# Performance work log

Hardware: AMD Instinct MI355X
Metric: run time of the kernel (lower is better)

## Reference

```python
import jax, jax.numpy as jnp
import numpy as np

N, F, HOPS, HID, NCLS = 100000, 128, 8, 256, 64

def prelu(x, a):
    return jnp.where(x >= 0, x, a * x)

def setup_inputs() -> dict:
    key = jax.random.key(0)
    ks = jax.random.split(key, 8)
    w = lambda i, shape: (jax.random.normal(ks[i], shape, dtype=jnp.float32) * 0.02)
    return {
        "feats": jax.random.normal(ks[0], (HOPS, N, F), dtype=jnp.float32),
        # lr_jk_ref: Dense(HOPS*F, HID) -> PReLU(a_jk) -> Dense(HID, HID)
        "W_jk1": w(1, (HOPS * F, HID)), "b_jk1": jnp.zeros((HID,), jnp.float32),
        "W_jk2": w(2, (HID, HID)),      "b_jk2": jnp.zeros((HID,), jnp.float32),
        # PReLU params (nn.PReLU default init 0.25): FFN-internal, module-level, output-FFN
        "a_jk": jnp.float32(0.25), "a_main": jnp.float32(0.25), "a_out": jnp.float32(0.25),
        # lr_att: Linear(HID + F, 1), split into the jk_ref part and the per-hop x part
        "w_att_ref": w(3, (HID,)), "w_att_x": w(4, (F,)), "b_att": jnp.zeros((), jnp.float32),
        # lr_output: Dense(F, HID) -> PReLU(a_out) -> Dense(HID, NCLS)
        "W_o1": w(5, (F, HID)),  "b_o1": jnp.zeros((HID,), jnp.float32),
        "W_o2": w(6, (HID, NCLS)), "b_o2": jnp.zeros((NCLS,), jnp.float32),
    }

def reference(feats, W_jk1, b_jk1, W_jk2, b_jk2, a_jk, a_main, a_out,
              w_att_ref, w_att_x, b_att, W_o1, b_o1, W_o2, b_o2):
    # feats: [HOPS, N, F]; dropouts are identity (rates = 0 / eval mode)
    n = feats.shape[1]
    # torch.cat(input_list, dim=1) -> [N, HOPS*F]
    concat = jnp.transpose(feats, (1, 0, 2)).reshape(n, -1)
    # lr_jk_ref (FeedForwardNetII, n_layers=2): Dense -> PReLU -> Dense, then module PReLU
    h = prelu(concat @ W_jk1 + b_jk1, a_jk)
    jk_ref = prelu(h @ W_jk2 + b_jk2, a_main)              # [N, HID]
    # attention scores: sigmoid(Linear(cat(jk_ref, x_i))) for each hop i, vectorized
    s_ref = jk_ref @ w_att_ref                              # [N]
    s_x = jnp.einsum('hnf,f->nh', feats, w_att_x)           # [N, HOPS]
    scores = jax.nn.sigmoid(s_x + s_ref[:, None] + b_att)   # [N, HOPS]
    Wsm = jax.nn.softmax(scores, axis=1)                    # softmax over hops
    # weighted multi-hop aggregation: sum_i W[:,i] * x_i
    agg = jnp.einsum('nh,hnf->nf', Wsm, feats)              # [N, F]
    # lr_output (FeedForwardNetII, n_layers=2): Dense -> PReLU -> Dense
    out = prelu(agg @ W_o1 + b_o1, a_out) @ W_o2 + b_o2     # [N, NCLS]
    return out
```

## Files before the change

### kernel.cpp

```cpp
#include <hip/hip_runtime.h>
#include <hip/hip_bf16.h>
#include <cstdint>
#include <cstddef>

#define N_F 128
#define N_HOPS 8
#define N_HID 256
#define N_CLS 64

typedef __bf16 bf16;
typedef __attribute__((ext_vector_type(8))) __bf16 bf16x8;
typedef __attribute__((ext_vector_type(4))) float f32x4;

__device__ inline f32x4 mfma16(bf16x8 a, bf16x8 b, f32x4 c) {
    return __builtin_amdgcn_mfma_f32_16x16x32_bf16(a, b, c, 0, 0, 0);
}

typedef const __attribute__((address_space(1))) unsigned int guint;
typedef __attribute__((address_space(3))) unsigned int luint;
__device__ __forceinline__ void gl_lds16(const void* g, void* l) {
    __builtin_amdgcn_global_load_lds((guint*)g, (luint*)l, 16, 0, 0);
}

__device__ inline void pack_one(const float* __restrict__ s, bf16* __restrict__ d,
                                int NC, int ntn, int idx) {
    const int lane = idx & 63;
    const int f = idx >> 6;
    const int kt = f / ntn, nt = f - kt * ntn;
    const int krow = kt * 32 + ((lane >> 4) << 3);
    const int col = nt * 16 + (lane & 15);
    const float* ss = s + (size_t)krow * NC + col;
    bf16* dd = d + ((size_t)f * 64 + lane) * 8;
#pragma unroll
    for (int j = 0; j < 8; ++j) dd[j] = (bf16)ss[(size_t)j * NC];
}

__global__ void pack_weights(const float* __restrict__ W1, const float* __restrict__ W2,
                             const float* __restrict__ O1, const float* __restrict__ O2,
                             bf16* p1, bf16* p2, bf16* p3, bf16* p4) {
    int i = blockIdx.x * 256 + threadIdx.x;
    if (i < 32768) { pack_one(W1, p1, 256, 16, i); return; }
    i -= 32768;
    if (i < 8192)  { pack_one(W2, p2, 256, 16, i); return; }
    i -= 8192;
    if (i < 4096)  { pack_one(O1, p3, 256, 16, i); return; }
    i -= 4096;
    if (i < 2048)  { pack_one(O2, p4, 64, 4, i); return; }
}

__global__ __launch_bounds__(256) void k1_kernel(
    const float* __restrict__ feats, const bf16* __restrict__ w1p, const bf16* __restrict__ w2p,
    const float* __restrict__ b1, const float* __restrict__ b2,
    const float* __restrict__ a_jk_p, const float* __restrict__ a_main_p,
    const float* __restrict__ wref, const float* __restrict__ wax,
    const float* __restrict__ batt_p,
    float* __restrict__ wsm, int N)
{
    union __align__(16) U1 {
        struct { bf16 A[2048]; bf16 B[8192]; } s;
        bf16 H[64 * 264];
    };
    __shared__ U1 u;
    __shared__ float sx[64 * 8];
    __shared__ float sref[64];

    const int t = threadIdx.x;
    const int lane = t & 63;
    const int wc = t >> 6;
    const int row0 = blockIdx.x * 64;

    for (int i = t; i < 64 * 8; i += 256) sx[i] = 0.f;
    if (t < 64) sref[t] = 0.f;
    __syncthreads();

    const int srow = t & 63;
    const int sc = t >> 6;
    const int grow = min(row0 + srow, N - 1);

    f32x4 acc[4][4] = {};
    float pacc = 0.f;

    for (int kt = 0; kt < 32; ++kt) {
        const int h = kt >> 2;
        const int f0 = ((kt & 3) << 5) + (sc << 3);
        const float* srcp = feats + ((size_t)h * N + grow) * N_F + f0;
        const float4 v0 = *(const float4*)srcp;
        const float4 v1 = *(const float4*)(srcp + 4);
        pacc += v0.x * wax[f0]     + v0.y * wax[f0 + 1] + v0.z * wax[f0 + 2] + v0.w * wax[f0 + 3]
              + v1.x * wax[f0 + 4] + v1.y * wax[f0 + 5] + v1.z * wax[f0 + 6] + v1.w * wax[f0 + 7];
        if ((kt & 3) == 3) { atomicAdd(&sx[srow * 8 + h], pacc); pacc = 0.f; }
        bf16x8 av;
        av[0] = (bf16)v0.x; av[1] = (bf16)v0.y; av[2] = (bf16)v0.z; av[3] = (bf16)v0.w;
        av[4] = (bf16)v1.x; av[5] = (bf16)v1.y; av[6] = (bf16)v1.z; av[7] = (bf16)v1.w;
        *(bf16x8*)&u.s.A[((((srow >> 4) << 6) + (sc << 4) + (srow & 15))) << 3] = av;
        const bf16* bsrc = w1p + (size_t)kt * 8192;
#pragma unroll
        for (int r = 0; r < 4; ++r)
            gl_lds16(bsrc + r * 2048 + t * 8, &u.s.B[r * 2048 + t * 8]);
        __syncthreads();
        bf16x8 af[4], bfr[4];
#pragma unroll
        for (int i = 0; i < 4; ++i) af[i] = *(bf16x8*)&u.s.A[((i << 6) + lane) << 3];
#pragma unroll
        for (int j = 0; j < 4; ++j) bfr[j] = *(bf16x8*)&u.s.B[(((wc << 2) + j) * 64 + lane) << 3];
#pragma unroll
        for (int i = 0; i < 4; ++i)
#pragma unroll
            for (int j = 0; j < 4; ++j)
                acc[i][j] = mfma16(af[i], bfr[j], acc[i][j]);
        __syncthreads();
    }

    const float ajk = *a_jk_p;
#pragma unroll
    for (int j = 0; j < 4; ++j) {
        const int colg = (wc << 6) + (j << 4) + (lane & 15);
        const float bias = b1[colg];
#pragma unroll
        for (int i = 0; i < 4; ++i)
#pragma unroll
            for (int r = 0; r < 4; ++r) {
                const int row = (i << 4) + ((lane >> 4) << 2) + r;
                float v = acc[i][j][r] + bias;
                v = v >= 0.f ? v : ajk * v;
                u.H[row * 264 + colg] = (bf16)v;
            }
    }
    __syncthreads();

    f32x4 acc2[4][4] = {};
    for (int kt = 0; kt < 8; ++kt) {
        bf16x8 af[4], bfr[4];
#pragma unroll
        for (int i = 0; i < 4; ++i)
            af[i] = *(bf16x8*)&u.H[((i << 4) + (lane & 15)) * 264 + (kt << 5) + ((lane >> 4) << 3)];
#pragma unroll
        for (int j = 0; j < 4; ++j)
            bfr[j] = *(const bf16x8*)&w2p[((size_t)((kt << 4) + (wc << 2) + j) * 64 + lane) * 8];
#pragma unroll
        for (int i = 0; i < 4; ++i)
#pragma unroll
            for (int j = 0; j < 4; ++j)
                acc2[i][j] = mfma16(af[i], bfr[j], acc2[i][j]);
    }

    const float amain = *a_main_p;
    float pr[4][4] = {};
#pragma unroll
    for (int j = 0; j < 4; ++j) {
        const int colg = (wc << 6) + (j << 4) + (lane & 15);
        const float bias = b2[colg];
        const float wr_ = wref[colg];
#pragma unroll
        for (int i = 0; i < 4; ++i)
#pragma unroll
            for (int r = 0; r < 4; ++r) {
                float v = acc2[i][j][r] + bias;
                v = v >= 0.f ? v : amain * v;
                pr[i][r] += v * wr_;
            }
    }
#pragma unroll
    for (int m = 1; m < 16; m <<= 1)
#pragma unroll
        for (int i = 0; i < 4; ++i)
#pragma unroll
            for (int r = 0; r < 4; ++r)
                pr[i][r] += __shfl_xor(pr[i][r], m, 64);
    if ((lane & 15) == 0) {
#pragma unroll
        for (int i = 0; i < 4; ++i)
#pragma unroll
            for (int r = 0; r < 4; ++r)
                atomicAdd(&sref[(i << 4) + ((lane >> 4) << 2) + r], pr[i][r]);
    }
    __syncthreads();

    if (t < 64) {
        const int rg = row0 + t;
        if (rg < N) {
            const float sr = sref[t] + *batt_p;
            float e[8], mx = -1e30f;
#pragma unroll
            for (int h = 0; h < 8; ++h) {
                const float s = 1.f / (1.f + expf(-(sx[t * 8 + h] + sr)));
                e[h] = s; mx = fmaxf(mx, s);
            }
            float sum = 0.f;
#pragma unroll
            for (int h = 0; h < 8; ++h) { e[h] = expf(e[h] - mx); sum += e[h]; }
            const float inv = 1.f / sum;
#pragma unroll
            for (int h = 0; h < 8; ++h) wsm[(size_t)rg * 8 + h] = e[h] * inv;
        }
    }
}

__global__ __launch_bounds__(256) void k2_kernel(
    const float* __restrict__ feats, const float* __restrict__ wsm,
    const bf16* __restrict__ o1p, const bf16* __restrict__ o2p,
    const float* __restrict__ bo1, const float* __restrict__ a_out_p,
    const float* __restrict__ bo2, float* __restrict__ out, int N)
{
    union __align__(16) U2 {
        bf16 AG[64 * 136];
        bf16 HO[64 * 264];
    };
    __shared__ U2 u;
    __shared__ float wsl[512];

    const int t = threadIdx.x;
    const int lane = t & 63;
    const int cg = t >> 6;
    const int row0 = blockIdx.x * 64;

    for (int i = t; i < 512; i += 256) {
        const int rg = min(row0 + (i >> 3), N - 1);
        wsl[i] = wsm[(size_t)rg * 8 + (i & 7)];
    }
    __syncthreads();

    {
        const int r = t >> 2;
        const int c = t & 3;
        const int rg = min(row0 + r, N - 1);
        f32x4 a4[8] = {};
#pragma unroll
        for (int h = 0; h < 8; ++h) {
            const float wgt = wsl[r * 8 + h];
            const f32x4* p4 = (const f32x4*)(feats + ((size_t)h * N + rg) * N_F + c * 32);
#pragma unroll
            for (int q = 0; q < 8; ++q) a4[q] += wgt * p4[q];
        }
#pragma unroll
        for (int q2 = 0; q2 < 4; ++q2) {
            bf16x8 av;
#pragma unroll
            for (int e = 0; e < 4; ++e) {
                av[e] = (bf16)a4[q2 * 2][e];
                av[4 + e] = (bf16)a4[q2 * 2 + 1][e];
            }
            *(bf16x8*)&u.AG[r * 136 + c * 32 + q2 * 8] = av;
        }
    }
    __syncthreads();

    f32x4 acc3[4][4] = {};
    for (int kt = 0; kt < 4; ++kt) {
        bf16x8 af[4], bfr[4];
#pragma unroll
        for (int i = 0; i < 4; ++i)
            af[i] = *(bf16x8*)&u.AG[((i << 4) + (lane & 15)) * 136 + (kt << 5) + ((lane >> 4) << 3)];
#pragma unroll
        for (int j = 0; j < 4; ++j)
            bfr[j] = *(const bf16x8*)&o1p[((size_t)((kt << 4) + (cg << 2) + j) * 64 + lane) * 8];
#pragma unroll
        for (int i = 0; i < 4; ++i)
#pragma unroll
            for (int j = 0; j < 4; ++j)
                acc3[i][j] = mfma16(af[i], bfr[j], acc3[i][j]);
    }
    __syncthreads();

    const float aout = *a_out_p;
#pragma unroll
    for (int j = 0; j < 4; ++j) {
        const int colg = (cg << 6) + (j << 4) + (lane & 15);
        const float bias = bo1[colg];
#pragma unroll
        for (int i = 0; i < 4; ++i)
#pragma unroll
            for (int r = 0; r < 4; ++r) {
                const int row = (i << 4) + ((lane >> 4) << 2) + r;
                float v = acc3[i][j][r] + bias;
                v = v >= 0.f ? v : aout * v;
                u.HO[row * 264 + colg] = (bf16)v;
            }
    }
    __syncthreads();

    f32x4 acc4[4] = {};
    for (int kt = 0; kt < 8; ++kt) {
        const bf16x8 b = *(const bf16x8*)&o2p[((size_t)((kt << 2) + cg) * 64 + lane) * 8];
#pragma unroll
        for (int i = 0; i < 4; ++i) {
            const bf16x8 a = *(bf16x8*)&u.HO[((i << 4) + (lane & 15)) * 264 + (kt << 5) + ((lane >> 4) << 3)];
            acc4[i] = mfma16(a, b, acc4[i]);
        }
    }
    {
        const int colg = (cg << 4) + (lane & 15);
        const float bv = bo2[colg];
#pragma unroll
        for (int i = 0; i < 4; ++i)
#pragma unroll
            for (int r = 0; r < 4; ++r) {
                const int rg = row0 + (i << 4) + ((lane >> 4) << 2) + r;
                if (rg < N) out[(size_t)rg * 64 + colg] = acc4[i][r] + bv;
            }
    }
}

extern "C" void kernel_launch(void* const* d_in, const int* in_sizes, int n_in,
                              void* d_out, int out_size, void* d_ws, size_t ws_size,
                              hipStream_t stream) {
    const float* feats  = (const float*)d_in[0];
    const float* W1     = (const float*)d_in[1];
    const float* b1     = (const float*)d_in[2];
    const float* W2     = (const float*)d_in[3];
    const float* b2     = (const float*)d_in[4];
    const float* a_jk   = (const float*)d_in[5];
    const float* a_main = (const float*)d_in[6];
    const float* a_out  = (const float*)d_in[7];
    const float* wref   = (const float*)d_in[8];
    const float* wax    = (const float*)d_in[9];
    const float* batt   = (const float*)d_in[10];
    const float* O1     = (const float*)d_in[11];
    const float* bo1    = (const float*)d_in[12];
    const float* O2     = (const float*)d_in[13];
    const float* bo2    = (const float*)d_in[14];

    const int N = in_sizes[0] / (N_HOPS * N_F);

    char* ws = (char*)d_ws;
    bf16* p1 = (bf16*)ws;
    bf16* p2 = (bf16*)(ws + 524288);
    bf16* p3 = (bf16*)(ws + 655360);
    bf16* p4 = (bf16*)(ws + 720896);
    float* wsm = (float*)(ws + 753664);

    pack_weights<<<184, 256, 0, stream>>>(W1, W2, O1, O2, p1, p2, p3, p4);
    const int nb = (N + 63) / 64;
    k1_kernel<<<nb, 256, 0, stream>>>(feats, p1, p2, b1, b2, a_jk, a_main,
                                      wref, wax, batt, wsm, N);
    k2_kernel<<<nb, 256, 0, stream>>>(feats, wsm, p3, p4, bo1, a_out, bo2,
                                      (float*)d_out, N);
}
```

Before: 771.9 us.

## Fuse attention and output kernels, double-buffer W1 tiles, repartition first GEMM by row

Merges the two per-row kernels into one, so the softmax hop weights stay in shared memory and the second pass over feats can hit cache soon after the first. The first GEMM now gives each wave 16 rows across all 256 columns, with A fragments loaded straight into registers. W1 tiles are double-buffered in LDS with the next tile prefetched, which drops one barrier per iteration. Hop scores are reduced with shuffles instead of shared atomics, and the aggregation loop prefetches the next hop. In exchange, each wave now reads all 16 B fragments per step, and register pressure and LDS footprint grow, which may lower occupancy.

```diff
diff --git a/kernel.cpp b/kernel.cpp
--- a/kernel.cpp
+++ b/kernel.cpp
@@ -48,107 +48,122 @@
     if (i < 2048)  { pack_one(O2, p4, 64, 4, i); return; }
 }
 
-__global__ __launch_bounds__(256) void k1_kernel(
+__global__ __launch_bounds__(256) void fused_kernel(
     const float* __restrict__ feats, const bf16* __restrict__ w1p, const bf16* __restrict__ w2p,
+    const bf16* __restrict__ o1p, const bf16* __restrict__ o2p,
     const float* __restrict__ b1, const float* __restrict__ b2,
     const float* __restrict__ a_jk_p, const float* __restrict__ a_main_p,
     const float* __restrict__ wref, const float* __restrict__ wax,
     const float* __restrict__ batt_p,
-    float* __restrict__ wsm, int N)
+    const float* __restrict__ bo1, const float* __restrict__ a_out_p,
+    const float* __restrict__ bo2, float* __restrict__ out, int N)
 {
-    union __align__(16) U1 {
-        struct { bf16 A[2048]; bf16 B[8192]; } s;
+    union __align__(16) U {
+        bf16 B[2][8192];
         bf16 H[64 * 264];
+        bf16 AG[64 * 136];
+        bf16 HO[64 * 264];
     };
-    __shared__ U1 u;
+    __shared__ U u;
     __shared__ float sx[64 * 8];
     __shared__ float sref[64];
 
     const int t = threadIdx.x;
     const int lane = t & 63;
-    const int wc = t >> 6;
+    const int wv = t >> 6;
     const int row0 = blockIdx.x * 64;
-
-    for (int i = t; i < 64 * 8; i += 256) sx[i] = 0.f;
+    const int rA = lane & 15;
+    const int cA = lane >> 4;
+
     if (t < 64) sref[t] = 0.f;
-    __syncthreads();
-
-    const int srow = t & 63;
-    const int sc = t >> 6;
-    const int grow = min(row0 + srow, N - 1);
-
-    f32x4 acc[4][4] = {};
+
+    const int growA = min(row0 + (wv << 4) + rA, N - 1);
+    const float* arow = feats + (size_t)growA * N_F + (cA << 3);
+    const size_t hopstride = (size_t)N * N_F;
+
+    f32x4 acc[16] = {};
     float pacc = 0.f;
 
+    float4 v0 = *(const float4*)(arow);
+    float4 v1 = *(const float4*)(arow + 4);
+#pragma unroll
+    for (int q = 0; q < 4; ++q)
+        gl_lds16(w1p + q * 2048 + t * 8, &u.B[0][q * 2048 + t * 8]);
+    __syncthreads();
+
+#pragma unroll 2
     for (int kt = 0; kt < 32; ++kt) {
-        const int h = kt >> 2;
-        const int f0 = ((kt & 3) << 5) + (sc << 3);
-        const float* srcp = feats + ((size_t)h * N + grow) * N_F + f0;
-        const float4 v0 = *(const float4*)srcp;
-        const float4 v1 = *(const float4*)(srcp + 4);
-        pacc += v0.x * wax[f0]     + v0.y * wax[f0 + 1] + v0.z * wax[f0 + 2] + v0.w * wax[f0 + 3]
-              + v1.x * wax[f0 + 4] + v1.y * wax[f0 + 5] + v1.z * wax[f0 + 6] + v1.w * wax[f0 + 7];
-        if ((kt & 3) == 3) { atomicAdd(&sx[srow * 8 + h], pacc); pacc = 0.f; }
-        bf16x8 av;
-        av[0] = (bf16)v0.x; av[1] = (bf16)v0.y; av[2] = (bf16)v0.z; av[3] = (bf16)v0.w;
-        av[4] = (bf16)v1.x; av[5] = (bf16)v1.y; av[6] = (bf16)v1.z; av[7] = (bf16)v1.w;
-        *(bf16x8*)&u.s.A[((((srow >> 4) << 6) + (sc << 4) + (srow & 15))) << 3] = av;
-        const bf16* bsrc = w1p + (size_t)kt * 8192;
-#pragma unroll
-        for (int r = 0; r < 4; ++r)
-            gl_lds16(bsrc + r * 2048 + t * 8, &u.s.B[r * 2048 + t * 8]);
+        const int cur = kt & 1;
+        float4 v0n, v1n;
+        if (kt < 31) {
+            const int kn = kt + 1;
+            const float* np = arow + (size_t)(kn >> 2) * hopstride + ((kn & 3) << 5);
+            v0n = *(const float4*)np;
+            v1n = *(const float4*)(np + 4);
+            const bf16* bsrc = w1p + (size_t)kn * 8192;
+#pragma unroll
+            for (int q = 0; q < 4; ++q)
+                gl_lds16(bsrc + q * 2048 + t * 8, &u.B[cur ^ 1][q * 2048 + t * 8]);
+        }
+        const int f0 = ((kt & 3) << 5) + (cA << 3);
+        const float4 wx0 = *(const float4*)&wax[f0];
+        const float4 wx1 = *(const float4*)&wax[f0 + 4];
+        pacc += v0.x * wx0.x + v0.y * wx0.y + v0.z * wx0.z + v0.w * wx0.w
+              + v1.x * wx1.x + v1.y * wx1.y + v1.z * wx1.z + v1.w * wx1.w;
+        if ((kt & 3) == 3) {
+            pacc += __shfl_xor(pacc, 16, 64);
+            pacc += __shfl_xor(pacc, 32, 64);
+            if (lane < 16) sx[(((wv << 4) + lane) << 3) + (kt >> 2)] = pacc;
+            pacc = 0.f;
+        }
+        bf16x8 af;
+        af[0] = (bf16)v0.x; af[1] = (bf16)v0.y; af[2] = (bf16)v0.z; af[3] = (bf16)v0.w;
+        af[4] = (bf16)v1.x; af[5] = (bf16)v1.y; af[6] = (bf16)v1.z; af[7] = (bf16)v1.w;
+#pragma unroll
+        for (int j = 0; j < 16; ++j) {
+            const bf16x8 bfr = *(const bf16x8*)&u.B[cur][((j << 6) + lane) << 3];
+            acc[j] = mfma16(af, bfr, acc[j]);
+        }
+        if (kt < 31) { v0 = v0n; v1 = v1n; }
         __syncthreads();
-        bf16x8 af[4], bfr[4];
-#pragma unroll
-        for (int i = 0; i < 4; ++i) af[i] = *(bf16x8*)&u.s.A[((i << 6) + lane) << 3];
-#pragma unroll
-        for (int j = 0; j < 4; ++j) bfr[j] = *(bf16x8*)&u.s.B[(((wc << 2) + j) * 64 + lane) << 3];
-#pragma unroll
-        for (int i = 0; i < 4; ++i)
-#pragma unroll
-            for (int j = 0; j < 4; ++j)
-                acc[i][j] = mfma16(af[i], bfr[j], acc[i][j]);
-        __syncthreads();
     }
 
     const float ajk = *a_jk_p;
 #pragma unroll
-    for (int j = 0; j < 4; ++j) {
-        const int colg = (wc << 6) + (j << 4) + (lane & 15);
+    for (int j = 0; j < 16; ++j) {
+        const int colg = (j << 4) + rA;
         const float bias = b1[colg];
 #pragma unroll
-        for (int i = 0; i < 4; ++i)
-#pragma unroll
-            for (int r = 0; r < 4; ++r) {
-                const int row = (i << 4) + ((lane >> 4) << 2) + r;
-                float v = acc[i][j][r] + bias;
-                v = v >= 0.f ? v : ajk * v;
-                u.H[row * 264 + colg] = (bf16)v;
-            }
+        for (int r = 0; r < 4; ++r) {
+            const int row = (wv << 4) + (cA << 2) + r;
+            float v = acc[j][r] + bias;
+            v = v >= 0.f ? v : ajk * v;
+            u.H[row * 264 + colg] = (bf16)v;
+        }
     }
     __syncthreads();
 
     f32x4 acc2[4][4] = {};
     for (int kt = 0; kt < 8; ++kt) {
-        bf16x8 af[4], bfr[4];
-#pragma unroll
-        for (int i = 0; i < 4; ++i)
-            af[i] = *(bf16x8*)&u.H[((i << 4) + (lane & 15)) * 264 + (kt << 5) + ((lane >> 4) << 3)];
+        bf16x8 af2[4], bfr[4];
+#pragma unroll
+        for (int i = 0; i < 4; ++i)
+            af2[i] = *(bf16x8*)&u.H[((i << 4) + rA) * 264 + (kt << 5) + (cA << 3)];
 #pragma unroll
         for (int j = 0; j < 4; ++j)
-            bfr[j] = *(const bf16x8*)&w2p[((size_t)((kt << 4) + (wc << 2) + j) * 64 + lane) * 8];
+            bfr[j] = *(const bf16x8*)&w2p[((size_t)((kt << 4) + (wv << 2) + j) * 64 + lane) * 8];
 #pragma unroll
         for (int i = 0; i < 4; ++i)
 #pragma unroll
             for (int j = 0; j < 4; ++j)
-                acc2[i][j] = mfma16(af[i], bfr[j], acc2[i][j]);
+                acc2[i][j] = mfma16(af2[i], bfr[j], acc2[i][j]);
     }
 
     const float amain = *a_main_p;
     float pr[4][4] = {};
 #pragma unroll
     for (int j = 0; j < 4; ++j) {
-        const int colg = (wc << 6) + (j << 4) + (lane & 15);
+        const int colg = (wv << 6) + (j << 4) + rA;
         const float bias = b2[colg];
         const float wr_ = wref[colg];
 #pragma unroll
@@ -167,56 +182,29 @@
 #pragma unroll
             for (int r = 0; r < 4; ++r)
                 pr[i][r] += __shfl_xor(pr[i][r], m, 64);
-    if ((lane & 15) == 0) {
+    if (rA == 0) {
 #pragma unroll
         for (int i = 0; i < 4; ++i)
 #pragma unroll
             for (int r = 0; r < 4; ++r)
-                atomicAdd(&sref[(i << 4) + ((lane >> 4) << 2) + r], pr[i][r]);
+                atomicAdd(&sref[(i << 4) + (cA << 2) + r], pr[i][r]);
     }
     __syncthreads();
 
     if (t < 64) {
-        const int rg = row0 + t;
-        if (rg < N) {
-            const float sr = sref[t] + *batt_p;
-            float e[8], mx = -1e30f;
-#pragma unroll
-            for (int h = 0; h < 8; ++h) {
-                const float s = 1.f / (1.f + expf(-(sx[t * 8 + h] + sr)));
-                e[h] = s; mx = fmaxf(mx, s);
-            }
-            float sum = 0.f;
-#pragma unroll
-            for (int h = 0; h < 8; ++h) { e[h] = expf(e[h] - mx); sum += e[h]; }
-            const float inv = 1.f / sum;
-#pragma unroll
-            for (int h = 0; h < 8; ++h) wsm[(size_t)rg * 8 + h] = e[h] * inv;
-        }
-    }
-}
-
-__global__ __launch_bounds__(256) void k2_kernel(
-    const float* __restrict__ feats, const float* __restrict__ wsm,
-    const bf16* __restrict__ o1p, const bf16* __restrict__ o2p,
-    const float* __restrict__ bo1, const float* __restrict__ a_out_p,
-    const float* __restrict__ bo2, float* __restrict__ out, int N)
-{
-    union __align__(16) U2 {
-        bf16 AG[64 * 136];
-        bf16 HO[64 * 264];
-    };
-    __shared__ U2 u;
-    __shared__ float wsl[512];
-
-    const int t = threadIdx.x;
-    const int lane = t & 63;
-    const int cg = t >> 6;
-    const int row0 = blockIdx.x * 64;
-
-    for (int i = t; i < 512; i += 256) {
-        const int rg = min(row0 + (i >> 3), N - 1);
-        wsl[i] = wsm[(size_t)rg * 8 + (i & 7)];
+        const float srf = sref[t] + *batt_p;
+        float e[8], mx = -1e30f;
+#pragma unroll
+        for (int h = 0; h < 8; ++h) {
+            const float s = 1.f / (1.f + expf(-(sx[(t << 3) + h] + srf)));
+            e[h] = s; mx = fmaxf(mx, s);
+        }
+        float sum = 0.f;
+#pragma unroll
+        for (int h = 0; h < 8; ++h) { e[h] = expf(e[h] - mx); sum += e[h]; }
+        const float inv = 1.f / sum;
+#pragma unroll
+        for (int h = 0; h < 8; ++h) sx[(t << 3) + h] = e[h] * inv;
     }
     __syncthreads();
 
@@ -224,54 +212,66 @@
         const int r = t >> 2;
         const int c = t & 3;
         const int rg = min(row0 + r, N - 1);
+        const float* bp = feats + (size_t)rg * N_F + (c << 5);
         f32x4 a4[8] = {};
+        f32x4 pA[8], pB[8];
+#pragma unroll
+        for (int q = 0; q < 8; ++q) pA[q] = ((const f32x4*)bp)[q];
 #pragma unroll
         for (int h = 0; h < 8; ++h) {
-            const float wgt = wsl[r * 8 + h];
-            const f32x4* p4 = (const f32x4*)(feats + ((size_t)h * N + rg) * N_F + c * 32);
-#pragma unroll
-            for (int q = 0; q < 8; ++q) a4[q] += wgt * p4[q];
+            if (h < 7) {
+                const f32x4* np = (const f32x4*)(bp + hopstride * (h + 1));
+#pragma unroll
+                for (int q = 0; q < 8; ++q) pB[q] = np[q];
+            }
+            const float wgt = sx[(r << 3) + h];
+#pragma unroll
+            for (int q = 0; q < 8; ++q) a4[q] += wgt * pA[q];
+            if (h < 7) {
+#pragma unroll
+                for (int q = 0; q < 8; ++q) pA[q] = pB[q];
+            }
         }
 #pragma unroll
         for (int q2 = 0; q2 < 4; ++q2) {
             bf16x8 av;
 #pragma unroll
-            for (int e = 0; e < 4; ++e) {
-                av[e] = (bf16)a4[q2 * 2][e];
-                av[4 + e] = (bf16)a4[q2 * 2 + 1][e];
-            }
-            *(bf16x8*)&u.AG[r * 136 + c * 32 + q2 * 8] = av;
+            for (int e2 = 0; e2 < 4; ++e2) {
+                av[e2] = (bf16)a4[q2 * 2][e2];
+                av[4 + e2] = (bf16)a4[q2 * 2 + 1][e2];
+            }
+            *(bf16x8*)&u.AG[r * 136 + (c << 5) + q2 * 8] = av;
         }
     }
     __syncthreads();
 
     f32x4 acc3[4][4] = {};
     for (int kt = 0; kt < 4; ++kt) {
-        bf16x8 af[4], bfr[4];
-#pragma unroll
-        for (int i = 0; i < 4; ++i)
-            af[i] = *(bf16x8*)&u.AG[((i << 4) + (lane & 15)) * 136 + (kt << 5) + ((lane >> 4) << 3)];
+        bf16x8 af3[4], bfr[4];
+#pragma unroll
+        for (int i = 0; i < 4; ++i)
+            af3[i] = *(bf16x8*)&u.AG[((i << 4) + rA) * 136 + (kt << 5) + (cA << 3)];
 #pragma unroll
         for (int j = 0; j < 4; ++j)
-            bfr[j] = *(const bf16x8*)&o1p[((size_t)((kt << 4) + (cg << 2) + j) * 64 + lane) * 8];
+            bfr[j] = *(const bf16x8*)&o1p[((size_t)((kt << 4) + (wv << 2) + j) * 64 + lane) * 8];
 #pragma unroll
         for (int i = 0; i < 4; ++i)
 #pragma unroll
             for (int j = 0; j < 4; ++j)
-                acc3[i][j] = mfma16(af[i], bfr[j], acc3[i][j]);
+                acc3[i][j] = mfma16(af3[i], bfr[j], acc3[i][j]);
     }
     __syncthreads();
 
     const float aout = *a_out_p;
 #pragma unroll
     for (int j = 0; j < 4; ++j) {
-        const int colg = (cg << 6) + (j << 4) + (lane & 15);
+        const int colg = (wv << 6) + (j << 4) + rA;
         const float bias = bo1[colg];
 #pragma unroll
         for (int i = 0; i < 4; ++i)
 #pragma unroll
             for (int r = 0; r < 4; ++r) {
-                const int row = (i << 4) + ((lane >> 4) << 2) + r;
+                const int row = (i << 4) + (cA << 2) + r;
                 float v = acc3[i][j][r] + bias;
                 v = v >= 0.f ? v : aout * v;
                 u.HO[row * 264 + colg] = (bf16)v;
@@ -281,21 +281,21 @@
 
     f32x4 acc4[4] = {};
     for (int kt = 0; kt < 8; ++kt) {
-        const bf16x8 b = *(const bf16x8*)&o2p[((size_t)((kt << 2) + cg) * 64 + lane) * 8];
+        const bf16x8 b = *(const bf16x8*)&o2p[((size_t)((kt << 2) + wv) * 64 + lane) * 8];
 #pragma unroll
         for (int i = 0; i < 4; ++i) {
-            const bf16x8 a = *(bf16x8*)&u.HO[((i << 4) + (lane & 15)) * 264 + (kt << 5) + ((lane >> 4) << 3)];
+            const bf16x8 a = *(bf16x8*)&u.HO[((i << 4) + rA) * 264 + (kt << 5) + (cA << 3)];
             acc4[i] = mfma16(a, b, acc4[i]);
         }
     }
     {
-        const int colg = (cg << 4) + (lane & 15);
+        const int colg = (wv << 4) + rA;
         const float bv = bo2[colg];
 #pragma unroll
         for (int i = 0; i < 4; ++i)
 #pragma unroll
             for (int r = 0; r < 4; ++r) {
-                const int rg = row0 + (i << 4) + ((lane >> 4) << 2) + r;
+                const int rg = row0 + (i << 4) + (cA << 2) + r;
                 if (rg < N) out[(size_t)rg * 64 + colg] = acc4[i][r] + bv;
             }
     }
@@ -327,12 +327,10 @@
     bf16* p2 = (bf16*)(ws + 524288);
     bf16* p3 = (bf16*)(ws + 655360);
     bf16* p4 = (bf16*)(ws + 720896);
-    float* wsm = (float*)(ws + 753664);
 
     pack_weights<<<184, 256, 0, stream>>>(W1, W2, O1, O2, p1, p2, p3, p4);
     const int nb = (N + 63) / 64;
-    k1_kernel<<<nb, 256, 0, stream>>>(feats, p1, p2, b1, b2, a_jk, a_main,
-                                      wref, wax, batt, wsm, N);
-    k2_kernel<<<nb, 256, 0, stream>>>(feats, wsm, p3, p4, bo1, a_out, bo2,
-                                      (float*)d_out, N);
-}
+    fused_kernel<<<nb, 256, 0, stream>>>(feats, p1, p2, p3, p4, b1, b2,
+                                         a_jk, a_main, wref, wax, batt,
+                                         bo1, a_out, bo2, (float*)d_out, N);
+}
```

After: 722.8 us. 1.07x faster.
